# Kernel optimization log

Measured on AMD Instinct MI355X. Metric: run time of the kernel, lower is better.

## Reference

```python
import jax, jax.numpy as jnp
import numpy as np

N = 6            # ensemble members (must match share_mode '6-1')
IN_C = 128
OUT_C = 128
K = 3
STRIDE = 1
PAD = 1
D = IN_C * OUT_C * K * K  # 147456
TEMP = 1.0
ZP1 = 1.2
ZP2 = -0.2
RES_DENOS = (3.0, 5.0)   # res_denos[:maxBWPow] with bw=2 -> [2**2-1, 2**2+1]


def round_ste(v):
    # straight-through round: forward round, backward identity
    return v + jax.lax.stop_gradient(jnp.round(v) - v)


def setup_inputs() -> dict:
    key = jax.random.key(0)
    k1, k2, k3, k4 = jax.random.split(key, 4)
    x = jax.random.normal(k1, (48, IN_C, 64, 64), jnp.float32)
    U = jax.random.normal(k2, (N, D), jnp.float32)
    bp = jax.random.normal(k3, (N + 1, D), jnp.float32)
    # uniform noise for the gumbel-sigmoid sample (open interval to avoid log(0))
    u = jax.random.uniform(k4, (N + 1, D), jnp.float32, 1e-6, 1.0 - 1e-6)
    return {"x": x, "U": U, "bp": bp, "u": u}


def reference(x, U, bp, u):
    beta = jnp.max(U)
    alpha = jnp.min(U)

    # gumbel-sigmoid gating
    g = jnp.log(u / (1.0 - u))
    bsamples = jax.nn.sigmoid((g + bp) / TEMP)
    gates = jnp.clip(bsamples * (ZP1 - ZP2) + ZP2, 0.0, 1.0)  # (7, D)
    # first 6 rows: per-member gates for level 0; last row shared across members for level 1
    gates = jnp.stack([gates[:N], jnp.broadcast_to(gates[N:], (N, D))], axis=0)  # (2, N, D)
    order_gates = jax.lax.stop_gradient(
        jnp.cumprod((gates > 0).astype(gates.dtype), axis=0)
    )

    # sequential residual-bit STE quantization (2 levels)
    s1 = (beta - alpha) / RES_DENOS[0]
    v1 = s1 * round_ste(U / s1)                       # (N, D)
    s2 = s1 / RES_DENOS[1]
    v2 = s2 * round_ste((U - v1.mean(0)) / s2)        # (N, D); vals.sum(0).mean(0) == v1.mean(0)
    vals = jnp.stack([v1, v2], axis=0)                # (2, N, D)

    w = (vals * (gates * order_gates)).sum(0)         # (N, D)
    w = w.reshape(OUT_C * N, IN_C, K, K)

    B = x.shape[0]
    xr = x.reshape(B // N, N * x.shape[1], x.shape[2], x.shape[3])
    act = jax.lax.conv_general_dilated(
        xr, w,
        window_strides=(STRIDE, STRIDE),
        padding=[(PAD, PAD), (PAD, PAD)],
        dimension_numbers=('NCHW', 'OIHW', 'NCHW'),
        feature_group_count=N,
    )
    return act.reshape(act.shape[0] * N, act.shape[1] // N, act.shape[2], act.shape[3])
```

## Files before the change

### kernel.cpp

```cpp
#include <hip/hip_runtime.h>
#include <stdint.h>

typedef __attribute__((ext_vector_type(8))) short bf16x8;
typedef __attribute__((ext_vector_type(4))) float f32x4;

#define DW 147456
#define NTOT (6 * DW)

__device__ __forceinline__ unsigned short f2bf(float f) {
    unsigned int u = __float_as_uint(f);
    u = (u + 0x7FFFu + ((u >> 16) & 1u)) >> 16;
    return (unsigned short)u;
}

__global__ __launch_bounds__(256) void reduce_part(const float* __restrict__ U,
                                                   float* __restrict__ part) {
    int tid = threadIdx.x;
    float mx = -INFINITY, mn = INFINITY;
    for (int i = blockIdx.x * 256 + tid; i < NTOT; i += 256 * 256) {
        float v = U[i];
        mx = fmaxf(mx, v);
        mn = fminf(mn, v);
    }
    __shared__ float smx[256], smn[256];
    smx[tid] = mx; smn[tid] = mn;
    __syncthreads();
    for (int s = 128; s > 0; s >>= 1) {
        if (tid < s) {
            smx[tid] = fmaxf(smx[tid], smx[tid + s]);
            smn[tid] = fminf(smn[tid], smn[tid + s]);
        }
        __syncthreads();
    }
    if (tid == 0) { part[blockIdx.x] = smx[0]; part[256 + blockIdx.x] = smn[0]; }
}

__global__ __launch_bounds__(256) void reduce_final(const float* __restrict__ part,
                                                    float* __restrict__ scal) {
    int tid = threadIdx.x;
    __shared__ float smx[256], smn[256];
    smx[tid] = part[tid]; smn[tid] = part[256 + tid];
    __syncthreads();
    for (int s = 128; s > 0; s >>= 1) {
        if (tid < s) {
            smx[tid] = fmaxf(smx[tid], smx[tid + s]);
            smn[tid] = fminf(smn[tid], smn[tid + s]);
        }
        __syncthreads();
    }
    if (tid == 0) { scal[0] = smx[0]; scal[1] = smn[0]; }
}

__global__ __launch_bounds__(256) void make_weights(const float* __restrict__ U,
                                                    const float* __restrict__ bp,
                                                    const float* __restrict__ uu,
                                                    const float* __restrict__ scal,
                                                    unsigned short* __restrict__ Wb2) {
    int d = blockIdx.x * 256 + threadIdx.x;
    if (d >= DW) return;
    float beta = scal[0], alpha = scal[1];
    float s1 = (beta - alpha) / 3.0f;
    float s2 = s1 / 5.0f;

    float v1[6]; float vsum = 0.f;
    #pragma unroll
    for (int n = 0; n < 6; n++) {
        float Un = U[n * DW + d];
        float v = s1 * rintf(Un / s1);
        v1[n] = v; vsum += v;
    }
    float vmean = vsum / 6.0f;

    float g6;
    {
        float un = uu[6 * DW + d];
        float g = logf(un / (1.0f - un));
        float sg = 1.0f / (1.0f + expf(-(g + bp[6 * DW + d])));
        g6 = fminf(fmaxf(sg * 1.4f - 0.2f, 0.0f), 1.0f);
    }

    int oc = d / 1152;
    int rem = d - oc * 1152;
    int ic = rem / 9;
    int t9 = rem - ic * 9;
    int c = ic >> 5, icc = ic & 31;
    size_t base = ((size_t)c * 9 + t9) * 4096 + (size_t)oc * 32 + icc;

    #pragma unroll
    for (int n = 0; n < 6; n++) {
        float un = uu[n * DW + d];
        float g = logf(un / (1.0f - un));
        float sg = 1.0f / (1.0f + expf(-(g + bp[n * DW + d])));
        float g0 = fminf(fmaxf(sg * 1.4f - 0.2f, 0.0f), 1.0f);
        float Un = U[n * DW + d];
        float v2 = s2 * rintf((Un - vmean) / s2);
        float w = v1[n] * g0 + ((g0 > 0.0f && g6 > 0.0f) ? v2 * g6 : 0.0f);
        Wb2[(size_t)n * DW + base] = f2bf(w);
    }
}

__global__ __launch_bounds__(256) void transform_x(const float* __restrict__ x,
                                                   unsigned short* __restrict__ xT) {
    __shared__ unsigned short Sh[128 * 70];
    int b = blockIdx.x;
    int img = b >> 6, row = b & 63;
    int tid = threadIdx.x;
    {
        int ch = tid >> 1;
        int col0 = (tid & 1) * 32;
        const float* src = x + (((size_t)(img * 128 + ch) * 64 + row) * 64 + col0);
        #pragma unroll
        for (int j = 0; j < 8; j++) {
            float4 v = ((const float4*)src)[j];
            unsigned int p0 = (unsigned int)f2bf(v.x) | ((unsigned int)f2bf(v.y) << 16);
            unsigned int p1 = (unsigned int)f2bf(v.z) | ((unsigned int)f2bf(v.w) << 16);
            unsigned int* dst = (unsigned int*)&Sh[ch * 70 + col0 + j * 4];
            dst[0] = p0; dst[1] = p1;
        }
    }
    __syncthreads();
    {
        int col = tid & 63;
        int chg = (tid >> 6) * 32;
        union { unsigned short s[32]; uint4 v[4]; } tmp;
        #pragma unroll
        for (int j = 0; j < 32; j++) tmp.s[j] = Sh[(chg + j) * 70 + col];
        uint4* dst = (uint4*)(xT + (((size_t)(img * 64 + row) * 64 + col) * 128 + chg));
        #pragma unroll
        for (int k = 0; k < 4; k++) dst[k] = tmp.v[k];
    }
}

__global__ __launch_bounds__(256) void conv_mfma(const unsigned short* __restrict__ xT,
                                                 const unsigned short* __restrict__ Wb2,
                                                 float* __restrict__ out) {
    __shared__ __align__(16) unsigned short Xs[4096];
    __shared__ __align__(16) unsigned short Ws[4096];
    int blk = blockIdx.x;
    int img = blk >> 5;
    int row0 = (blk & 31) * 2;
    int mem = img - (img / 6) * 6;
    const unsigned short* Wsrc = Wb2 + (size_t)mem * DW;
    const unsigned short* Xsrc = xT + (size_t)img * 524288;

    int tid = threadIdx.x;
    int lane = tid & 63;
    int wave = tid >> 6;
    int ocbase = (wave & 1) * 64;
    int pxbase = (wave >> 1) * 64;
    int lr = lane & 15, lq = lane >> 4;

    f32x4 acc[4][4];
    #pragma unroll
    for (int mi = 0; mi < 4; mi++)
        #pragma unroll
        for (int ni = 0; ni < 4; ni++)
            acc[mi][ni] = (f32x4){0.f, 0.f, 0.f, 0.f};

    for (int c = 0; c < 4; c++) {
        for (int t = 0; t < 9; t++) {
            int dy = t / 3;
            int dx = t - dy * 3;
            #pragma unroll
            for (int ii = 0; ii < 2; ii++) {
                int i = tid + ii * 256;
                int px = i >> 2, cc = i & 3;
                int srow = row0 + (px >> 6) + dy - 1;
                int scol = (px & 63) + dx - 1;
                uint4 v = make_uint4(0u, 0u, 0u, 0u);
                if ((unsigned)srow < 64u && (unsigned)scol < 64u)
                    v = *(const uint4*)(Xsrc + ((srow * 64 + scol) * 128 + c * 32 + cc * 8));
                *(uint4*)(Xs + i * 8) = v;
            }
            const unsigned short* wp = Wsrc + (c * 9 + t) * 4096;
            #pragma unroll
            for (int ii = 0; ii < 2; ii++) {
                int i = tid + ii * 256;
                *(uint4*)(Ws + i * 8) = *(const uint4*)(wp + i * 8);
            }
            __syncthreads();
            bf16x8 af[4], bfr[4];
            #pragma unroll
            for (int mi = 0; mi < 4; mi++)
                af[mi] = *(const bf16x8*)(Ws + (ocbase + mi * 16 + lr) * 32 + lq * 8);
            #pragma unroll
            for (int ni = 0; ni < 4; ni++)
                bfr[ni] = *(const bf16x8*)(Xs + (pxbase + ni * 16 + lr) * 32 + lq * 8);
            #pragma unroll
            for (int mi = 0; mi < 4; mi++)
                #pragma unroll
                for (int ni = 0; ni < 4; ni++)
                    acc[mi][ni] = __builtin_amdgcn_mfma_f32_16x16x32_bf16(
                        af[mi], bfr[ni], acc[mi][ni], 0, 0, 0);
            __syncthreads();
        }
    }
    float* obase = out + (size_t)img * 524288 + row0 * 64;
    #pragma unroll
    for (int mi = 0; mi < 4; mi++) {
        #pragma unroll
        for (int ni = 0; ni < 4; ni++) {
            int px = pxbase + ni * 16 + lr;
            int ocb = ocbase + mi * 16 + lq * 4;
            #pragma unroll
            for (int rr = 0; rr < 4; rr++)
                obase[(size_t)(ocb + rr) * 4096 + px] = acc[mi][ni][rr];
        }
    }
}

extern "C" void kernel_launch(void* const* d_in, const int* in_sizes, int n_in,
                              void* d_out, int out_size, void* d_ws, size_t ws_size,
                              hipStream_t stream) {
    const float* x  = (const float*)d_in[0];
    const float* U  = (const float*)d_in[1];
    const float* bp = (const float*)d_in[2];
    const float* uu = (const float*)d_in[3];
    float* out = (float*)d_out;

    char* ws = (char*)d_ws;
    float* part = (float*)ws;
    float* scal = (float*)(ws + 2048);
    unsigned short* Wb2 = (unsigned short*)(ws + 4096);
    unsigned short* xT  = (unsigned short*)(ws + 4096 + 1769472);

    reduce_part <<<256, 256, 0, stream>>>(U, part);
    reduce_final<<<1, 256, 0, stream>>>(part, scal);
    make_weights<<<576, 256, 0, stream>>>(U, bp, uu, scal, Wb2);
    transform_x <<<48 * 64, 256, 0, stream>>>(x, xT);
    conv_mfma   <<<48 * 32, 256, 0, stream>>>(xT, Wb2, out);
}
```

Before: 313.6 us.

## Restage conv with halo LDS tiles, direct global-to-LDS loads, fused reductions

The conv kernel now stages a 6-row haloed input band and all 9 tap weights per channel chunk into LDS using global_load_lds. The 9 taps then reuse that band through shifted LDS reads instead of re-fetching input per tap, which cuts global traffic and per-tap barriers. Each block now covers 4 rows × 64 oc rather than 2 rows × 128 oc. Separately, the x transform switches to a channel-chunk-major layout, the min/max reduction is vectorised and its final stage fused into make_weights, and the gumbel-sigmoid is simplified algebraically. The trade-off is larger LDS usage and a different tile shape with less output-channel reuse per block.

```diff
diff --git a/kernel.cpp b/kernel.cpp
--- a/kernel.cpp
+++ b/kernel.cpp
@@ -17,10 +17,11 @@
                                                    float* __restrict__ part) {
     int tid = threadIdx.x;
     float mx = -INFINITY, mn = INFINITY;
-    for (int i = blockIdx.x * 256 + tid; i < NTOT; i += 256 * 256) {
-        float v = U[i];
-        mx = fmaxf(mx, v);
-        mn = fminf(mn, v);
+    const float4* U4 = (const float4*)U;
+    for (int i = blockIdx.x * 256 + tid; i < NTOT / 4; i += 256 * 256) {
+        float4 v = U4[i];
+        mx = fmaxf(fmaxf(fmaxf(mx, v.x), v.y), fmaxf(v.z, v.w));
+        mn = fminf(fminf(fminf(mn, v.x), v.y), fminf(v.z, v.w));
     }
     __shared__ float smx[256], smn[256];
     smx[tid] = mx; smn[tid] = mn;
@@ -35,8 +36,11 @@
     if (tid == 0) { part[blockIdx.x] = smx[0]; part[256 + blockIdx.x] = smn[0]; }
 }
 
-__global__ __launch_bounds__(256) void reduce_final(const float* __restrict__ part,
-                                                    float* __restrict__ scal) {
+__global__ __launch_bounds__(256) void make_weights(const float* __restrict__ U,
+                                                    const float* __restrict__ bp,
+                                                    const float* __restrict__ uu,
+                                                    const float* __restrict__ part,
+                                                    unsigned short* __restrict__ Wb2) {
     int tid = threadIdx.x;
     __shared__ float smx[256], smn[256];
     smx[tid] = part[tid]; smn[tid] = part[256 + tid];
@@ -48,24 +52,17 @@
         }
         __syncthreads();
     }
-    if (tid == 0) { scal[0] = smx[0]; scal[1] = smn[0]; }
-}
-
-__global__ __launch_bounds__(256) void make_weights(const float* __restrict__ U,
-                                                    const float* __restrict__ bp,
-                                                    const float* __restrict__ uu,
-                                                    const float* __restrict__ scal,
-                                                    unsigned short* __restrict__ Wb2) {
-    int d = blockIdx.x * 256 + threadIdx.x;
-    if (d >= DW) return;
-    float beta = scal[0], alpha = scal[1];
+    float beta = smx[0], alpha = smn[0];
     float s1 = (beta - alpha) / 3.0f;
     float s2 = s1 / 5.0f;
 
-    float v1[6]; float vsum = 0.f;
+    int d = blockIdx.x * 256 + tid;
+
+    float v1[6]; float Uv[6]; float vsum = 0.f;
     #pragma unroll
     for (int n = 0; n < 6; n++) {
         float Un = U[n * DW + d];
+        Uv[n] = Un;
         float v = s1 * rintf(Un / s1);
         v1[n] = v; vsum += v;
     }
@@ -74,8 +71,7 @@
     float g6;
     {
         float un = uu[6 * DW + d];
-        float g = logf(un / (1.0f - un));
-        float sg = 1.0f / (1.0f + expf(-(g + bp[6 * DW + d])));
+        float sg = un / (un + (1.0f - un) * expf(-bp[6 * DW + d]));
         g6 = fminf(fmaxf(sg * 1.4f - 0.2f, 0.0f), 1.0f);
     }
 
@@ -89,11 +85,9 @@
     #pragma unroll
     for (int n = 0; n < 6; n++) {
         float un = uu[n * DW + d];
-        float g = logf(un / (1.0f - un));
-        float sg = 1.0f / (1.0f + expf(-(g + bp[n * DW + d])));
+        float sg = un / (un + (1.0f - un) * expf(-bp[n * DW + d]));
         float g0 = fminf(fmaxf(sg * 1.4f - 0.2f, 0.0f), 1.0f);
-        float Un = U[n * DW + d];
-        float v2 = s2 * rintf((Un - vmean) / s2);
+        float v2 = s2 * rintf((Uv[n] - vmean) / s2);
         float w = v1[n] * g0 + ((g0 > 0.0f && g6 > 0.0f) ? v2 * g6 : 0.0f);
         Wb2[(size_t)n * DW + base] = f2bf(w);
     }
@@ -121,34 +115,61 @@
     __syncthreads();
     {
         int col = tid & 63;
-        int chg = (tid >> 6) * 32;
+        int q = tid >> 6;
+        int chg = q * 32;
         union { unsigned short s[32]; uint4 v[4]; } tmp;
         #pragma unroll
         for (int j = 0; j < 32; j++) tmp.s[j] = Sh[(chg + j) * 70 + col];
-        uint4* dst = (uint4*)(xT + (((size_t)(img * 64 + row) * 64 + col) * 128 + chg));
+        uint4* dst = (uint4*)(xT + ((size_t)img * 524288 + (size_t)q * 131072 +
+                                    (size_t)row * 2048 + col * 32));
         #pragma unroll
         for (int k = 0; k < 4; k++) dst[k] = tmp.v[k];
     }
 }
+
+typedef const __attribute__((address_space(1))) void CGV;
+typedef __attribute__((address_space(3))) void LV;
 
 __global__ __launch_bounds__(256) void conv_mfma(const unsigned short* __restrict__ xT,
                                                  const unsigned short* __restrict__ Wb2,
                                                  float* __restrict__ out) {
-    __shared__ __align__(16) unsigned short Xs[4096];
-    __shared__ __align__(16) unsigned short Ws[4096];
+    __shared__ __align__(16) unsigned short Xs[6 * 66 * 32];
+    __shared__ __align__(16) unsigned short Ws[9 * 64 * 32];
     int blk = blockIdx.x;
+    int band = blk & 15;
+    int och = (blk >> 4) & 1;
     int img = blk >> 5;
-    int row0 = (blk & 31) * 2;
+    int row0 = band * 4;
     int mem = img - (img / 6) * 6;
-    const unsigned short* Wsrc = Wb2 + (size_t)mem * DW;
+    const unsigned short* Wsrc = Wb2 + (size_t)mem * DW + och * 2048;
     const unsigned short* Xsrc = xT + (size_t)img * 524288;
 
     int tid = threadIdx.x;
     int lane = tid & 63;
-    int wave = tid >> 6;
-    int ocbase = (wave & 1) * 64;
-    int pxbase = (wave >> 1) * 64;
+    int prow = tid >> 6;
     int lr = lane & 15, lq = lane >> 4;
+
+    if (tid < 192) {
+        int r = tid >> 5, j = tid & 31;
+        int col = (j < 16) ? 0 : 65;
+        *(unsigned int*)&Xs[(r * 66 + col) * 32 + (j & 15) * 2] = 0u;
+    }
+
+    auto stage = [&](int c) {
+        #pragma unroll
+        for (int t = 0; t < 9; t++)
+            __builtin_amdgcn_global_load_lds((CGV*)(Wsrc + (c * 9 + t) * 4096 + tid * 8),
+                                             (LV*)(&Ws[t * 2048 + tid * 8]), 16, 0, 0);
+        #pragma unroll
+        for (int r = 0; r < 6; r++) {
+            int srow = row0 + r - 1;
+            if ((unsigned)srow < 64u)
+                __builtin_amdgcn_global_load_lds((CGV*)(Xsrc + c * 131072 + srow * 2048 + tid * 8),
+                                                 (LV*)(&Xs[(r * 66 + 1) * 32 + tid * 8]), 16, 0, 0);
+            else
+                *(uint4*)&Xs[(r * 66 + 1) * 32 + tid * 8] = make_uint4(0u, 0u, 0u, 0u);
+        }
+    };
 
     f32x4 acc[4][4];
     #pragma unroll
@@ -157,51 +178,41 @@
         for (int ni = 0; ni < 4; ni++)
             acc[mi][ni] = (f32x4){0.f, 0.f, 0.f, 0.f};
 
+    stage(0);
+    __syncthreads();
+
     for (int c = 0; c < 4; c++) {
+        #pragma unroll
         for (int t = 0; t < 9; t++) {
-            int dy = t / 3;
-            int dx = t - dy * 3;
-            #pragma unroll
-            for (int ii = 0; ii < 2; ii++) {
-                int i = tid + ii * 256;
-                int px = i >> 2, cc = i & 3;
-                int srow = row0 + (px >> 6) + dy - 1;
-                int scol = (px & 63) + dx - 1;
-                uint4 v = make_uint4(0u, 0u, 0u, 0u);
-                if ((unsigned)srow < 64u && (unsigned)scol < 64u)
-                    v = *(const uint4*)(Xsrc + ((srow * 64 + scol) * 128 + c * 32 + cc * 8));
-                *(uint4*)(Xs + i * 8) = v;
-            }
-            const unsigned short* wp = Wsrc + (c * 9 + t) * 4096;
-            #pragma unroll
-            for (int ii = 0; ii < 2; ii++) {
-                int i = tid + ii * 256;
-                *(uint4*)(Ws + i * 8) = *(const uint4*)(wp + i * 8);
-            }
-            __syncthreads();
+            int dy = t / 3, dx = t - dy * 3;
             bf16x8 af[4], bfr[4];
             #pragma unroll
             for (int mi = 0; mi < 4; mi++)
-                af[mi] = *(const bf16x8*)(Ws + (ocbase + mi * 16 + lr) * 32 + lq * 8);
+                af[mi] = *(const bf16x8*)(&Ws[t * 2048 + (mi * 16 + lr) * 32 + lq * 8]);
             #pragma unroll
             for (int ni = 0; ni < 4; ni++)
-                bfr[ni] = *(const bf16x8*)(Xs + (pxbase + ni * 16 + lr) * 32 + lq * 8);
+                bfr[ni] = *(const bf16x8*)(&Xs[((prow + dy) * 66 + ni * 16 + lr + dx) * 32 + lq * 8]);
             #pragma unroll
             for (int mi = 0; mi < 4; mi++)
                 #pragma unroll
                 for (int ni = 0; ni < 4; ni++)
                     acc[mi][ni] = __builtin_amdgcn_mfma_f32_16x16x32_bf16(
                         af[mi], bfr[ni], acc[mi][ni], 0, 0, 0);
+        }
+        if (c < 3) {
             __syncthreads();
-        }
-    }
-    float* obase = out + (size_t)img * 524288 + row0 * 64;
+            stage(c + 1);
+            __syncthreads();
+        }
+    }
+
+    float* obase = out + (size_t)img * 524288 + (size_t)(row0 + prow) * 64;
     #pragma unroll
     for (int mi = 0; mi < 4; mi++) {
         #pragma unroll
         for (int ni = 0; ni < 4; ni++) {
-            int px = pxbase + ni * 16 + lr;
-            int ocb = ocbase + mi * 16 + lq * 4;
+            int px = ni * 16 + lr;
+            int ocb = och * 64 + mi * 16 + lq * 4;
             #pragma unroll
             for (int rr = 0; rr < 4; rr++)
                 obase[(size_t)(ocb + rr) * 4096 + px] = acc[mi][ni][rr];
@@ -220,13 +231,11 @@
 
     char* ws = (char*)d_ws;
     float* part = (float*)ws;
-    float* scal = (float*)(ws + 2048);
     unsigned short* Wb2 = (unsigned short*)(ws + 4096);
     unsigned short* xT  = (unsigned short*)(ws + 4096 + 1769472);
 
     reduce_part <<<256, 256, 0, stream>>>(U, part);
-    reduce_final<<<1, 256, 0, stream>>>(part, scal);
-    make_weights<<<576, 256, 0, stream>>>(U, bp, uu, scal, Wb2);
+    make_weights<<<576, 256, 0, stream>>>(U, bp, uu, part, Wb2);
     transform_x <<<48 * 64, 256, 0, stream>>>(x, xT);
     conv_mfma   <<<48 * 32, 256, 0, stream>>>(xT, Wb2, out);
 }
```

Result: faster. 253.5 us (-19.2%).
